# Optimization experiments

Measured on AMD Instinct MI355X. Metric: run time of the kernel, lower is better.

## Reference

```python
import jax, jax.numpy as jnp
import numpy as np

WINDOW = 25          # window_size -> h = w = 25, n = 625 tokens
DIM = 512
DIM_HEAD = 64
HEADS = DIM // DIM_HEAD
BATCH = 64


def _rel_pos_indices(ws):
    # mirrors the torch buffer: pairwise relative offsets on a ws x ws grid
    pos = np.arange(ws)
    gi, gj = np.meshgrid(pos, pos, indexing='ij')
    grid = np.stack([gi.reshape(-1), gj.reshape(-1)], axis=-1)      # (ws*ws, 2)
    rel = grid[:, None, :] - grid[None, :, :] + (ws - 1)            # (n, n, 2)
    return (rel[..., 0] * (2 * ws - 1) + rel[..., 1]).astype(np.int32)


def setup_inputs() -> dict:
    key = jax.random.key(0)
    k1, k2, k3, k4 = jax.random.split(key, 4)
    x = jax.random.normal(k1, (BATCH, DIM, WINDOW, WINDOW), jnp.float32)
    w_qkv = jax.random.normal(k2, (DIM, 3 * DIM), jnp.float32) * 0.02   # to_qkv weight (x @ w_qkv)
    w_out = jax.random.normal(k3, (DIM, DIM), jnp.float32) * 0.02       # to_out weight
    rel_pos_bias = jax.random.normal(k4, ((2 * WINDOW - 1) ** 2, HEADS), jnp.float32) * 0.02
    rel_pos_indices = jnp.asarray(_rel_pos_indices(WINDOW))
    return {"x": x, "w_qkv": w_qkv, "w_out": w_out,
            "rel_pos_bias": rel_pos_bias, "rel_pos_indices": rel_pos_indices}


def reference(x, w_qkv, w_out, rel_pos_bias, rel_pos_indices):
    b, d, h, w = x.shape
    n = h * w
    dh = DIM_HEAD
    m = d // dh
    scale = dh ** -0.5
    tokens = x.reshape(b, d, n).transpose(0, 2, 1)                  # b n d
    qkv = tokens @ w_qkv                                            # b n 3d
    q, k, v = jnp.split(qkv, 3, axis=-1)
    split_heads = lambda t: t.reshape(b, n, m, dh).transpose(0, 2, 1, 3)  # b m n dh
    q = split_heads(q) * scale
    k = split_heads(k)
    v = split_heads(v)
    sim = jnp.einsum('bmid,bmjd->bmij', q, k)                       # b m n n
    bias = rel_pos_bias[rel_pos_indices]                            # n n m  (embedding lookup)
    sim = sim + bias.transpose(2, 0, 1)[None]                       # add rel-pos bias inline
    attn = jax.nn.softmax(sim, axis=-1)
    out = jnp.einsum('bmij,bmjd->bmid', attn, v)                    # b m n dh
    out = out.transpose(0, 2, 1, 3).reshape(b, n, m * dh)           # concat heads
    out = out @ w_out                                               # b n d
    return out.transpose(0, 2, 1).reshape(b, d, h, w)
```

## Files before the change

kernel.cpp:

```cpp
#include <hip/hip_runtime.h>
#include <cstdint>
#include <cstddef>

typedef unsigned short u16;
typedef __attribute__((ext_vector_type(8))) short bf16x8;
typedef __attribute__((ext_vector_type(4))) float f32x4;

#define NB    64
#define NTOK  625
#define NTOKP 640
#define DDIM  512
#define NH    8
#define DH    64

__device__ __forceinline__ float bf2f(u16 v) {
    return __uint_as_float(((unsigned int)v) << 16);
}
__device__ __forceinline__ u16 f2bf(float f) {
    unsigned int x = __float_as_uint(f);
    unsigned int r = (x + 0x7fffu + ((x >> 16) & 1u)) >> 16;
    return (u16)r;
}
__device__ __forceinline__ u16 f2bf_fast(float f) {
    return (u16)((__float_as_uint(f) + 0x8000u) >> 16);
}

#if __has_builtin(__builtin_amdgcn_global_load_lds)
typedef const __attribute__((address_space(1))) void gas_void;
typedef __attribute__((address_space(3))) void las_void;
__device__ __forceinline__ void glds16(const void* g, void* l) {
    __builtin_amdgcn_global_load_lds((gas_void*)g, (las_void*)l, 16, 0, 0);
}
#else
__device__ __forceinline__ void glds16(const void* g, void* l) {
    *(uint4*)l = *(const uint4*)g;
}
#endif

__global__ __launch_bounds__(256) void k_transpose_x(const float* __restrict__ x,
                                                     u16* __restrict__ tokens) {
    __shared__ u16 T[64][66];
    int b = blockIdx.z, ct = blockIdx.y, it = blockIdx.x;
    int t = threadIdx.x;
    int i0 = it * 64, c0 = ct * 64;
#pragma unroll
    for (int r = 0; r < 2; r++) {
        int c = (t >> 3) + r * 32;
        int i8 = (t & 7) * 8;
        const float* s = x + ((size_t)b * DDIM + c0 + c) * NTOK + i0 + i8;
#pragma unroll
        for (int u = 0; u < 8; u++)
            T[c][i8 + u] = (i0 + i8 + u < NTOK) ? f2bf(s[u]) : (u16)0;
    }
    __syncthreads();
#pragma unroll
    for (int r = 0; r < 2; r++) {
        int i = (t >> 3) + r * 32;
        int c8 = (t & 7) * 8;
        int gi = i0 + i;
        u16* d = tokens + ((size_t)b * NTOKP + gi) * DDIM + c0 + c8;
#pragma unroll
        for (int u = 0; u < 8; u++) d[u] = T[c8 + u][i];
    }
}

__global__ __launch_bounds__(256) void k_transpose_w(const float* __restrict__ src,
                                                     u16* __restrict__ dst, int R, int C) {
    __shared__ u16 T[64][66];
    int r0 = blockIdx.y * 64, c0 = blockIdx.x * 64;
    int t = threadIdx.x;
#pragma unroll
    for (int rr = 0; rr < 2; rr++) {
        int r = (t >> 3) + rr * 32;
        int c8 = (t & 7) * 8;
        const float* s = src + (size_t)(r0 + r) * C + c0 + c8;
#pragma unroll
        for (int u = 0; u < 8; u++) T[r][c8 + u] = f2bf(s[u]);
    }
    __syncthreads();
#pragma unroll
    for (int rr = 0; rr < 2; rr++) {
        int c = (t >> 3) + rr * 32;
        int r8 = (t & 7) * 8;
        u16* d = dst + (size_t)(c0 + c) * R + r0 + r8;
#pragma unroll
        for (int u = 0; u < 8; u++) d[u] = T[r8 + u][c];
    }
}

__global__ __launch_bounds__(256) void k_bias(const int* __restrict__ rpi,
                                              const float* __restrict__ rpb,
                                              float* __restrict__ biasCf) {
    int blk = blockIdx.x;
    int m = blk / 100, jt = (blk / 10) % 10, it = blk % 10;
    int t = threadIdx.x;
    float vals[16];
#pragma unroll
    for (int jj = 0; jj < 4; jj++) {
        int gj = jt * 64 + jj * 16 + (t & 15);
#pragma unroll
        for (int r = 0; r < 4; r++) {
            int gi = it * 64 + (t >> 6) * 16 + ((t >> 4) & 3) * 4 + r;
            float v;
            if (gj >= NTOK) v = -1e30f;
            else if (gi >= NTOK) v = 0.f;
            else v = rpb[rpi[gi * NTOK + gj] * NH + m];
            vals[jj * 4 + r] = v;
        }
    }
    float* d = biasCf + ((size_t)(m * 10 + jt) * 10 + it) * 4096 + t * 16;
#pragma unroll
    for (int g = 0; g < 4; g++)
        *(f32x4*)(d + g * 4) = *(f32x4*)&vals[g * 4];
}

__global__ __launch_bounds__(256, 4) void k_qkv(const u16* __restrict__ tokens,
                                                const u16* __restrict__ wT,
                                                u16* __restrict__ qk, u16* __restrict__ vT) {
    __shared__ u16 SMEM[9216];
    int bid = blockIdx.x;
    int c8id = bid & 7, t2 = bid >> 3;
    int jt = t2 % 12, q_ = t2 / 12;
    int itb = q_ * 8 + c8id;
    int it = itb % 5, b = itb / 5;
    int i0 = it * 128, j0 = jt * 128;
    int t = threadIdx.x;
    int w = t >> 6, lane = t & 63, quad = lane >> 4, l15 = lane & 15;
    int wr = w >> 1, wc = w & 1;
    int swl = (l15 + (l15 >> 2)) & 3;
    f32x4 acc[4][4] = {};
    const u16* abase = tokens + ((size_t)b * NTOKP + i0) * DDIM;
    const u16* bbase = wT + (size_t)j0 * DDIM;
    for (int k0 = 0; k0 < DDIM; k0 += 32) {
        __syncthreads();
#pragma unroll
        for (int c = 0; c < 2; c++) {
            int unit = c * 256 + t;
            int row = unit >> 2, cc = unit & 3;
            int gcol = (cc ^ ((row + (row >> 2)) & 3)) * 8;
            glds16(abase + (size_t)row * DDIM + k0 + gcol, SMEM + unit * 8);
            glds16(bbase + (size_t)row * DDIM + k0 + gcol, SMEM + 4096 + unit * 8);
        }
        __syncthreads();
        bf16x8 af[4], bfv[4];
        int chA = (quad ^ swl) * 8;
#pragma unroll
        for (int q2 = 0; q2 < 4; q2++) {
            af[q2]  = *(const bf16x8*)&SMEM[(wr * 64 + q2 * 16 + l15) * 32 + chA];
            bfv[q2] = *(const bf16x8*)&SMEM[4096 + (wc * 64 + q2 * 16 + l15) * 32 + chA];
        }
#pragma unroll
        for (int ii = 0; ii < 4; ii++)
#pragma unroll
            for (int jj = 0; jj < 4; jj++)
                acc[ii][jj] = __builtin_amdgcn_mfma_f32_16x16x32_bf16(af[ii], bfv[jj], acc[ii][jj], 0, 0, 0);
    }
    __syncthreads();
    if (jt < 8) {
        float scale = (j0 < 512) ? 0.125f : 1.0f;
#pragma unroll
        for (int h = 0; h < 2; h++) {
            if (h) __syncthreads();
            if (wr == h) {
#pragma unroll
                for (int ii = 0; ii < 4; ii++)
#pragma unroll
                    for (int jj = 0; jj < 4; jj++)
#pragma unroll
                        for (int r = 0; r < 4; r++)
                            SMEM[(ii * 16 + quad * 4 + r) * 136 + wc * 64 + jj * 16 + l15] =
                                f2bf(acc[ii][jj][r] * scale);
            }
            __syncthreads();
#pragma unroll
            for (int g = 0; g < 4; g++) {
                int unit = g * 256 + t;
                int tok = unit >> 4, ch8 = (unit & 15) * 8;
                *(uint4*)(qk + ((size_t)b * NTOKP + i0 + h * 64 + tok) * 1024 + j0 + ch8) =
                    *(uint4*)&SMEM[tok * 136 + ch8];
            }
        }
    } else {
        int ch0 = j0 - 1024;
#pragma unroll
        for (int h = 0; h < 2; h++) {
            if (h) __syncthreads();
            if (wr == h) {
#pragma unroll
                for (int ii = 0; ii < 4; ii++)
#pragma unroll
                    for (int jj = 0; jj < 4; jj++)
#pragma unroll
                        for (int r = 0; r < 4; r++) {
                            int tok = ii * 16 + quad * 4 + r;
                            SMEM[(wc * 64 + jj * 16 + l15) * 72 + (tok & 15) * 4 + (tok >> 4)] =
                                f2bf(acc[ii][jj][r]);
                        }
            }
            __syncthreads();
#pragma unroll
            for (int g = 0; g < 4; g++) {
                int unit = g * 256 + t;
                int chl = unit >> 3, tok8 = (unit & 7) * 8;
                int chv = ch0 + chl, hd = chv >> 6, tc = chv & 63;
                *(uint4*)(vT + (((size_t)b * NH + hd) * DH + tc) * NTOKP + i0 + h * 64 + tok8) =
                    *(uint4*)&SMEM[chl * 72 + tok8];
            }
        }
    }
}

__global__ __launch_bounds__(256) void k_attn(const u16* __restrict__ qk,
                                              const u16* __restrict__ vT,
                                              const float* __restrict__ biasCf,
                                              u16* __restrict__ attnout) {
    __shared__ u16 Qs[64][72];
    __shared__ u16 Ks[64][72];
    __shared__ u16 Vs[80][72];
    __shared__ u16 Ps[64][72];
    int bid = blockIdx.x;
    int c8id = bid & 7, t2 = bid >> 3;
    int it = t2 % 10, q_ = t2 / 10;
    int bm = q_ * 8 + c8id;
    int m = bm & 7, b = bm >> 3;
    int i0 = it * 64;
    int t = threadIdx.x;
    int w = t >> 6, lane = t & 63, quad = lane >> 4, l15 = lane & 15;
    {
        int row = 64 + (t >> 4), c4 = (t & 15) * 4;
        *(uint2*)&Vs[row][c4] = make_uint2(0x3F803F80u, 0x3F803F80u);
    }
#pragma unroll
    for (int r = 0; r < 2; r++) {
        int row = (t >> 3) + r * 32;
        int t8 = (t & 7) * 8;
        *(uint4*)&Qs[row][t8] =
            *(const uint4*)(qk + ((size_t)b * NTOKP + i0 + row) * 1024 + m * DH + t8);
    }
    __syncthreads();
    bf16x8 aq[2], vones[2];
#pragma unroll
    for (int kk = 0; kk < 2; kk++) {
        aq[kk]    = *(const bf16x8*)&Qs[w * 16 + l15][kk * 32 + quad * 8];
        vones[kk] = *(const bf16x8*)&Vs[64 + l15][kk * 32 + quad * 8];
    }
    f32x4 oacc[5] = {};
    const u16* vbase = vT + ((size_t)b * NH + m) * DH * NTOKP;
    const float* bC = biasCf + (size_t)(m * 100 + it) * 4096 + t * 16;

    for (int jt = 0; jt < 10; jt++) {
        int j0 = jt * 64;
        __syncthreads();
#pragma unroll
        for (int r = 0; r < 2; r++) {
            int row = (t >> 3) + r * 32;
            int c8 = (t & 7) * 8;
            *(uint4*)&Ks[row][c8] =
                *(const uint4*)(qk + ((size_t)b * NTOKP + j0 + row) * 1024 + 512 + m * DH + c8);
            *(uint4*)&Vs[row][c8] = *(const uint4*)(vbase + (size_t)row * NTOKP + j0 + c8);
        }
        __syncthreads();
        const float* bp = bC + (size_t)jt * 10 * 4096;
        f32x4 s[4];
#pragma unroll
        for (int jj = 0; jj < 4; jj++) s[jj] = *(const f32x4*)(bp + jj * 4);
#pragma unroll
        for (int jj = 0; jj < 4; jj++)
#pragma unroll
            for (int kk = 0; kk < 2; kk++) {
                bf16x8 bk = *(const bf16x8*)&Ks[jj * 16 + l15][kk * 32 + quad * 8];
                s[jj] = __builtin_amdgcn_mfma_f32_16x16x32_bf16(aq[kk], bk, s[jj], 0, 0, 0);
            }
#pragma unroll
        for (int r = 0; r < 4; r++) {
            float p0 = __expf(s[0][r]), p1 = __expf(s[1][r]);
            float p2 = __expf(s[2][r]), p3 = __expf(s[3][r]);
            uint2 pk;
            pk.x = (unsigned)f2bf_fast(p0) | ((unsigned)f2bf_fast(p1) << 16);
            pk.y = (unsigned)f2bf_fast(p2) | ((unsigned)f2bf_fast(p3) << 16);
            *(uint2*)&Ps[w * 16 + quad * 4 + r][l15 * 4] = pk;
        }
        bf16x8 ap[2];
#pragma unroll
        for (int kk = 0; kk < 2; kk++)
            ap[kk] = *(const bf16x8*)&Ps[w * 16 + l15][kk * 32 + quad * 8];
#pragma unroll
        for (int tt = 0; tt < 4; tt++)
#pragma unroll
            for (int kk = 0; kk < 2; kk++) {
                bf16x8 bv = *(const bf16x8*)&Vs[tt * 16 + l15][kk * 32 + quad * 8];
                oacc[tt] = __builtin_amdgcn_mfma_f32_16x16x32_bf16(ap[kk], bv, oacc[tt], 0, 0, 0);
            }
#pragma unroll
        for (int kk = 0; kk < 2; kk++)
            oacc[4] = __builtin_amdgcn_mfma_f32_16x16x32_bf16(ap[kk], vones[kk], oacc[4], 0, 0, 0);
    }
    float rinv[4];
#pragma unroll
    for (int r = 0; r < 4; r++) rinv[r] = __frcp_rn(oacc[4][r]);
#pragma unroll
    for (int tt = 0; tt < 4; tt++)
#pragma unroll
        for (int r = 0; r < 4; r++) {
            int gi = i0 + w * 16 + quad * 4 + r;
            if (gi < NTOK)
                attnout[((size_t)b * NTOKP + gi) * DDIM + m * DH + tt * 16 + l15] =
                    f2bf(oacc[tt][r] * rinv[r]);
        }
}

__global__ __launch_bounds__(256, 4) void k_out(const u16* __restrict__ attnout,
                                                const u16* __restrict__ woT,
                                                float* __restrict__ out) {
    __shared__ u16 SMEM[8192];
    int bid = blockIdx.x;
    int c8id = bid & 7, t2 = bid >> 3;
    int jt = t2 % 4, q_ = t2 / 4;
    int itb = q_ * 8 + c8id;
    int it = itb % 5, b = itb / 5;
    int j0 = jt * 128, i0 = it * 128;
    int t = threadIdx.x;
    int w = t >> 6, lane = t & 63, quad = lane >> 4, l15 = lane & 15;
    int wr = w >> 1, wc = w & 1;
    int swl = (l15 + (l15 >> 2)) & 3;
    f32x4 acc[4][4] = {};
    const u16* abase = woT + (size_t)j0 * DDIM;
    const u16* bbase = attnout + ((size_t)b * NTOKP + i0) * DDIM;
    for (int k0 = 0; k0 < DDIM; k0 += 32) {
        __syncthreads();
#pragma unroll
        for (int c = 0; c < 2; c++) {
            int unit = c * 256 + t;
            int row = unit >> 2, cc = unit & 3;
            int gcol = (cc ^ ((row + (row >> 2)) & 3)) * 8;
            glds16(abase + (size_t)row * DDIM + k0 + gcol, SMEM + unit * 8);
            glds16(bbase + (size_t)row * DDIM + k0 + gcol, SMEM + 4096 + unit * 8);
        }
        __syncthreads();
        bf16x8 af[4], bfv[4];
        int chA = (quad ^ swl) * 8;
#pragma unroll
        for (int q2 = 0; q2 < 4; q2++) {
            af[q2]  = *(const bf16x8*)&SMEM[(wr * 64 + q2 * 16 + l15) * 32 + chA];
            bfv[q2] = *(const bf16x8*)&SMEM[4096 + (wc * 64 + q2 * 16 + l15) * 32 + chA];
        }
#pragma unroll
        for (int ii = 0; ii < 4; ii++)
#pragma unroll
            for (int jj = 0; jj < 4; jj++)
                acc[ii][jj] = __builtin_amdgcn_mfma_f32_16x16x32_bf16(af[ii], bfv[jj], acc[ii][jj], 0, 0, 0);
    }
#pragma unroll
    for (int ii = 0; ii < 4; ii++)
#pragma unroll
        for (int jj = 0; jj < 4; jj++) {
            int gi = i0 + wc * 64 + jj * 16 + l15;
            if (gi >= NTOK) continue;
#pragma unroll
            for (int r = 0; r < 4; r++) {
                int gj = j0 + wr * 64 + ii * 16 + quad * 4 + r;
                out[((size_t)b * DDIM + gj) * NTOK + gi] = acc[ii][jj][r];
            }
        }
}

extern "C" void kernel_launch(void* const* d_in, const int* in_sizes, int n_in,
                              void* d_out, int out_size, void* d_ws, size_t ws_size,
                              hipStream_t stream) {
    const float* x    = (const float*)d_in[0];
    const float* wqkv = (const float*)d_in[1];
    const float* wout = (const float*)d_in[2];
    const float* rpb  = (const float*)d_in[3];
    const int*   rpi  = (const int*)d_in[4];
    float* out = (float*)d_out;

    char* ws = (char*)d_ws;
    size_t off = 0;
    auto alloc = [&](size_t nbytes) -> void* {
        void* p = ws + off;
        off += (nbytes + 255) & ~(size_t)255;
        return p;
    };
    u16* tokens   = (u16*)alloc((size_t)NB * NTOKP * DDIM * 2);
    u16* qk       = (u16*)alloc((size_t)NB * NTOKP * 1024 * 2);
    u16* vT       = (u16*)alloc((size_t)NB * NH * DH * NTOKP * 2);
    u16* wqkvT    = (u16*)alloc((size_t)1536 * DDIM * 2);
    u16* woutT    = (u16*)alloc((size_t)DDIM * DDIM * 2);
    float* biasCf = (float*)alloc((size_t)NH * 100 * 4096 * 4);
    u16* attnout  = tokens;

    k_transpose_x<<<dim3(10, 8, NB), 256, 0, stream>>>(x, tokens);
    k_transpose_w<<<dim3(1536 / 64, DDIM / 64), 256, 0, stream>>>(wqkv, wqkvT, DDIM, 1536);
    k_transpose_w<<<dim3(DDIM / 64, DDIM / 64), 256, 0, stream>>>(wout, woutT, DDIM, DDIM);
    k_bias<<<dim3(800), 256, 0, stream>>>(rpi, rpb, biasCf);
    k_qkv<<<dim3(3840), 256, 0, stream>>>(tokens, wqkvT, qk, vT);
    k_attn<<<dim3(5120), 256, 0, stream>>>(qk, vT, biasCf, attnout);
    k_out<<<dim3(1280), 256, 0, stream>>>(attnout, woutT, out);
}
```

Baseline: 419.5 us.

## Double-buffer LDS loads in GEMMs and attention, use exp2 with prescaled log2e

```diff
diff --git a/kernel.cpp b/kernel.cpp
--- a/kernel.cpp
+++ b/kernel.cpp
@@ -12,6 +12,7 @@
 #define DDIM  512
 #define NH    8
 #define DH    64
+#define LOG2E 1.44269504088896f
 
 __device__ __forceinline__ float bf2f(u16 v) {
     return __uint_as_float(((unsigned int)v) << 16);
@@ -21,8 +22,21 @@
     unsigned int r = (x + 0x7fffu + ((x >> 16) & 1u)) >> 16;
     return (u16)r;
 }
-__device__ __forceinline__ u16 f2bf_fast(float f) {
-    return (u16)((__float_as_uint(f) + 0x8000u) >> 16);
+__device__ __forceinline__ float fexp2(float x) {
+#if __has_builtin(__builtin_amdgcn_exp2f)
+    return __builtin_amdgcn_exp2f(x);
+#else
+    return exp2f(x);
+#endif
+}
+__device__ __forceinline__ unsigned pack_bf16(float a, float b) {
+#if __has_builtin(__builtin_amdgcn_perm)
+    return __builtin_amdgcn_perm(__float_as_uint(b) + 0x8000u,
+                                 __float_as_uint(a) + 0x8000u, 0x07060302u);
+#else
+    return ((__float_as_uint(a) + 0x8000u) >> 16) |
+           (((__float_as_uint(b) + 0x8000u) >> 16) << 16);
+#endif
 }
 
 #if __has_builtin(__builtin_amdgcn_global_load_lds)
@@ -105,7 +119,7 @@
             if (gj >= NTOK) v = -1e30f;
             else if (gi >= NTOK) v = 0.f;
             else v = rpb[rpi[gi * NTOK + gj] * NH + m];
-            vals[jj * 4 + r] = v;
+            vals[jj * 4 + r] = v * LOG2E;
         }
     }
     float* d = biasCf + ((size_t)(m * 10 + jt) * 10 + it) * 4096 + t * 16;
@@ -117,7 +131,7 @@
 __global__ __launch_bounds__(256, 4) void k_qkv(const u16* __restrict__ tokens,
                                                 const u16* __restrict__ wT,
                                                 u16* __restrict__ qk, u16* __restrict__ vT) {
-    __shared__ u16 SMEM[9216];
+    __shared__ u16 SMEM[16384];
     int bid = blockIdx.x;
     int c8id = bid & 7, t2 = bid >> 3;
     int jt = t2 % 12, q_ = t2 / 12;
@@ -128,36 +142,40 @@
     int w = t >> 6, lane = t & 63, quad = lane >> 4, l15 = lane & 15;
     int wr = w >> 1, wc = w & 1;
     int swl = (l15 + (l15 >> 2)) & 3;
-    f32x4 acc[4][4] = {};
     const u16* abase = tokens + ((size_t)b * NTOKP + i0) * DDIM;
     const u16* bbase = wT + (size_t)j0 * DDIM;
-    for (int k0 = 0; k0 < DDIM; k0 += 32) {
-        __syncthreads();
+    auto stage = [&](int k0, int buf) {
 #pragma unroll
         for (int c = 0; c < 2; c++) {
             int unit = c * 256 + t;
             int row = unit >> 2, cc = unit & 3;
             int gcol = (cc ^ ((row + (row >> 2)) & 3)) * 8;
-            glds16(abase + (size_t)row * DDIM + k0 + gcol, SMEM + unit * 8);
-            glds16(bbase + (size_t)row * DDIM + k0 + gcol, SMEM + 4096 + unit * 8);
-        }
-        __syncthreads();
+            glds16(abase + (size_t)row * DDIM + k0 + gcol, SMEM + buf * 4096 + unit * 8);
+            glds16(bbase + (size_t)row * DDIM + k0 + gcol, SMEM + 8192 + buf * 4096 + unit * 8);
+        }
+    };
+    stage(0, 0);
+    __syncthreads();
+    f32x4 acc[4][4] = {};
+    for (int k0 = 0; k0 < DDIM; k0 += 32) {
+        int pc = (k0 >> 5) & 1;
+        if (k0 + 32 < DDIM) stage(k0 + 32, pc ^ 1);
         bf16x8 af[4], bfv[4];
         int chA = (quad ^ swl) * 8;
 #pragma unroll
         for (int q2 = 0; q2 < 4; q2++) {
-            af[q2]  = *(const bf16x8*)&SMEM[(wr * 64 + q2 * 16 + l15) * 32 + chA];
-            bfv[q2] = *(const bf16x8*)&SMEM[4096 + (wc * 64 + q2 * 16 + l15) * 32 + chA];
+            af[q2]  = *(const bf16x8*)&SMEM[pc * 4096 + (wr * 64 + q2 * 16 + l15) * 32 + chA];
+            bfv[q2] = *(const bf16x8*)&SMEM[8192 + pc * 4096 + (wc * 64 + q2 * 16 + l15) * 32 + chA];
         }
 #pragma unroll
         for (int ii = 0; ii < 4; ii++)
 #pragma unroll
             for (int jj = 0; jj < 4; jj++)
                 acc[ii][jj] = __builtin_amdgcn_mfma_f32_16x16x32_bf16(af[ii], bfv[jj], acc[ii][jj], 0, 0, 0);
-    }
-    __syncthreads();
+        __syncthreads();
+    }
     if (jt < 8) {
-        float scale = (j0 < 512) ? 0.125f : 1.0f;
+        float scale = (j0 < 512) ? 0.125f * LOG2E : 1.0f;
 #pragma unroll
         for (int h = 0; h < 2; h++) {
             if (h) __syncthreads();
@@ -210,14 +228,11 @@
     }
 }
 
-__global__ __launch_bounds__(256) void k_attn(const u16* __restrict__ qk,
-                                              const u16* __restrict__ vT,
-                                              const float* __restrict__ biasCf,
-                                              u16* __restrict__ attnout) {
-    __shared__ u16 Qs[64][72];
-    __shared__ u16 Ks[64][72];
-    __shared__ u16 Vs[80][72];
-    __shared__ u16 Ps[64][72];
+__global__ __launch_bounds__(256, 3) void k_attn(const u16* __restrict__ qk,
+                                                 const u16* __restrict__ vT,
+                                                 const float* __restrict__ biasCf,
+                                                 u16* __restrict__ attnout) {
+    __shared__ u16 S[25088];
     int bid = blockIdx.x;
     int c8id = bid & 7, t2 = bid >> 3;
     int it = t2 % 10, q_ = t2 / 10;
@@ -226,74 +241,96 @@
     int i0 = it * 64;
     int t = threadIdx.x;
     int w = t >> 6, lane = t & 63, quad = lane >> 4, l15 = lane & 15;
-    {
-        int row = 64 + (t >> 4), c4 = (t & 15) * 4;
-        *(uint2*)&Vs[row][c4] = make_uint2(0x3F803F80u, 0x3F803F80u);
-    }
-#pragma unroll
-    for (int r = 0; r < 2; r++) {
-        int row = (t >> 3) + r * 32;
-        int t8 = (t & 7) * 8;
-        *(uint4*)&Qs[row][t8] =
-            *(const uint4*)(qk + ((size_t)b * NTOKP + i0 + row) * 1024 + m * DH + t8);
-    }
+
+    const u16* qbase = qk + ((size_t)b * NTOKP + i0) * 1024 + m * DH;
+    const u16* kbase = qk + (size_t)b * NTOKP * 1024 + 512 + m * DH;
+    const u16* vbase = vT + ((size_t)b * NH + m) * DH * NTOKP;
+
+#pragma unroll
+    for (int c = 0; c < 2; c++) {
+        int unit = c * 256 + t;
+        int row = unit >> 3, pch = unit & 7;
+        int gcol = (pch ^ (row & 7)) * 8;
+        glds16(qbase + (size_t)row * 1024 + gcol, S + unit * 8);
+    }
+#pragma unroll
+    for (int c = 0; c < 2; c++) {
+        int unit = c * 256 + t;
+        int row = unit >> 3, pch = unit & 7;
+        int gcol = (pch ^ (row & 7)) * 8;
+        glds16(kbase + (size_t)row * 1024 + gcol, S + 4096 + unit * 8);
+        glds16(vbase + (size_t)row * NTOKP + gcol, S + 12288 + unit * 8);
+    }
+    const float* bC = biasCf + (size_t)(m * 100 + it) * 4096 + t * 16;
+    f32x4 ba[2][4];
+#pragma unroll
+    for (int jj = 0; jj < 4; jj++) ba[0][jj] = *(const f32x4*)(bC + jj * 4);
     __syncthreads();
-    bf16x8 aq[2], vones[2];
-#pragma unroll
-    for (int kk = 0; kk < 2; kk++) {
-        aq[kk]    = *(const bf16x8*)&Qs[w * 16 + l15][kk * 32 + quad * 8];
-        vones[kk] = *(const bf16x8*)&Vs[64 + l15][kk * 32 + quad * 8];
-    }
+
+    bf16x8 aq[2];
+#pragma unroll
+    for (int kk = 0; kk < 2; kk++)
+        aq[kk] = *(const bf16x8*)&S[(w * 16 + l15) * 64 + ((4 * kk + quad) ^ (l15 & 7)) * 8];
+    bf16x8 vone;
+#pragma unroll
+    for (int e = 0; e < 8; e++) vone[e] = (short)0x3F80;
+
     f32x4 oacc[5] = {};
-    const u16* vbase = vT + ((size_t)b * NH + m) * DH * NTOKP;
-    const float* bC = biasCf + (size_t)(m * 100 + it) * 4096 + t * 16;
-
+#pragma unroll
     for (int jt = 0; jt < 10; jt++) {
-        int j0 = jt * 64;
+        int p = jt & 1;
+        if (jt < 9) {
+            const float* bp = bC + (size_t)(jt + 1) * 40960;
+#pragma unroll
+            for (int jj = 0; jj < 4; jj++) ba[p ^ 1][jj] = *(const f32x4*)(bp + jj * 4);
+            int j1 = (jt + 1) * 64;
+#pragma unroll
+            for (int c = 0; c < 2; c++) {
+                int unit = c * 256 + t;
+                int row = unit >> 3, pch = unit & 7;
+                int gcol = (pch ^ (row & 7)) * 8;
+                glds16(kbase + (size_t)(j1 + row) * 1024 + gcol,
+                       S + 4096 + (p ^ 1) * 4096 + unit * 8);
+                glds16(vbase + (size_t)row * NTOKP + j1 + gcol,
+                       S + 12288 + (p ^ 1) * 4096 + unit * 8);
+            }
+        }
+        f32x4 s[4];
+#pragma unroll
+        for (int jj = 0; jj < 4; jj++) s[jj] = ba[p][jj];
+#pragma unroll
+        for (int jj = 0; jj < 4; jj++)
+#pragma unroll
+            for (int kk = 0; kk < 2; kk++) {
+                bf16x8 bk = *(const bf16x8*)&S[4096 + p * 4096 + (jj * 16 + l15) * 64 +
+                                               ((4 * kk + quad) ^ (l15 & 7)) * 8];
+                s[jj] = __builtin_amdgcn_mfma_f32_16x16x32_bf16(aq[kk], bk, s[jj], 0, 0, 0);
+            }
+#pragma unroll
+        for (int r = 0; r < 4; r++) {
+            float p0 = fexp2(s[0][r]), p1 = fexp2(s[1][r]);
+            float p2 = fexp2(s[2][r]), p3 = fexp2(s[3][r]);
+            uint2 pk;
+            pk.x = pack_bf16(p0, p1);
+            pk.y = pack_bf16(p2, p3);
+            *(uint2*)&S[20480 + (w * 16 + quad * 4 + r) * 72 + l15 * 4] = pk;
+        }
+        bf16x8 ap[2];
+#pragma unroll
+        for (int kk = 0; kk < 2; kk++)
+            ap[kk] = *(const bf16x8*)&S[20480 + (w * 16 + l15) * 72 + kk * 32 + quad * 8];
+#pragma unroll
+        for (int tt = 0; tt < 4; tt++)
+#pragma unroll
+            for (int kk = 0; kk < 2; kk++) {
+                bf16x8 bv = *(const bf16x8*)&S[12288 + p * 4096 + (tt * 16 + l15) * 64 +
+                                               ((4 * kk + quad) ^ (l15 & 7)) * 8];
+                oacc[tt] = __builtin_amdgcn_mfma_f32_16x16x32_bf16(ap[kk], bv, oacc[tt], 0, 0, 0);
+            }
+#pragma unroll
+        for (int kk = 0; kk < 2; kk++)
+            oacc[4] = __builtin_amdgcn_mfma_f32_16x16x32_bf16(ap[kk], vone, oacc[4], 0, 0, 0);
         __syncthreads();
-#pragma unroll
-        for (int r = 0; r < 2; r++) {
-            int row = (t >> 3) + r * 32;
-            int c8 = (t & 7) * 8;
-            *(uint4*)&Ks[row][c8] =
-                *(const uint4*)(qk + ((size_t)b * NTOKP + j0 + row) * 1024 + 512 + m * DH + c8);
-            *(uint4*)&Vs[row][c8] = *(const uint4*)(vbase + (size_t)row * NTOKP + j0 + c8);
-        }
-        __syncthreads();
-        const float* bp = bC + (size_t)jt * 10 * 4096;
-        f32x4 s[4];
-#pragma unroll
-        for (int jj = 0; jj < 4; jj++) s[jj] = *(const f32x4*)(bp + jj * 4);
-#pragma unroll
-        for (int jj = 0; jj < 4; jj++)
-#pragma unroll
-            for (int kk = 0; kk < 2; kk++) {
-                bf16x8 bk = *(const bf16x8*)&Ks[jj * 16 + l15][kk * 32 + quad * 8];
-                s[jj] = __builtin_amdgcn_mfma_f32_16x16x32_bf16(aq[kk], bk, s[jj], 0, 0, 0);
-            }
-#pragma unroll
-        for (int r = 0; r < 4; r++) {
-            float p0 = __expf(s[0][r]), p1 = __expf(s[1][r]);
-            float p2 = __expf(s[2][r]), p3 = __expf(s[3][r]);
-            uint2 pk;
-            pk.x = (unsigned)f2bf_fast(p0) | ((unsigned)f2bf_fast(p1) << 16);
-            pk.y = (unsigned)f2bf_fast(p2) | ((unsigned)f2bf_fast(p3) << 16);
-            *(uint2*)&Ps[w * 16 + quad * 4 + r][l15 * 4] = pk;
-        }
-        bf16x8 ap[2];
-#pragma unroll
-        for (int kk = 0; kk < 2; kk++)
-            ap[kk] = *(const bf16x8*)&Ps[w * 16 + l15][kk * 32 + quad * 8];
-#pragma unroll
-        for (int tt = 0; tt < 4; tt++)
-#pragma unroll
-            for (int kk = 0; kk < 2; kk++) {
-                bf16x8 bv = *(const bf16x8*)&Vs[tt * 16 + l15][kk * 32 + quad * 8];
-                oacc[tt] = __builtin_amdgcn_mfma_f32_16x16x32_bf16(ap[kk], bv, oacc[tt], 0, 0, 0);
-            }
-#pragma unroll
-        for (int kk = 0; kk < 2; kk++)
-            oacc[4] = __builtin_amdgcn_mfma_f32_16x16x32_bf16(ap[kk], vones[kk], oacc[4], 0, 0, 0);
     }
     float rinv[4];
 #pragma unroll
@@ -312,7 +349,7 @@
 __global__ __launch_bounds__(256, 4) void k_out(const u16* __restrict__ attnout,
                                                 const u16* __restrict__ woT,
                                                 float* __restrict__ out) {
-    __shared__ u16 SMEM[8192];
+    __shared__ u16 SMEM[16384];
     int bid = blockIdx.x;
     int c8id = bid & 7, t2 = bid >> 3;
     int jt = t2 % 4, q_ = t2 / 4;
@@ -323,32 +360,37 @@
     int w = t >> 6, lane = t & 63, quad = lane >> 4, l15 = lane & 15;
     int wr = w >> 1, wc = w & 1;
     int swl = (l15 + (l15 >> 2)) & 3;
-    f32x4 acc[4][4] = {};
     const u16* abase = woT + (size_t)j0 * DDIM;
     const u16* bbase = attnout + ((size_t)b * NTOKP + i0) * DDIM;
-    for (int k0 = 0; k0 < DDIM; k0 += 32) {
-        __syncthreads();
+    auto stage = [&](int k0, int buf) {
 #pragma unroll
         for (int c = 0; c < 2; c++) {
             int unit = c * 256 + t;
             int row = unit >> 2, cc = unit & 3;
             int gcol = (cc ^ ((row + (row >> 2)) & 3)) * 8;
-            glds16(abase + (size_t)row * DDIM + k0 + gcol, SMEM + unit * 8);
-            glds16(bbase + (size_t)row * DDIM + k0 + gcol, SMEM + 4096 + unit * 8);
-        }
-        __syncthreads();
+            glds16(abase + (size_t)row * DDIM + k0 + gcol, SMEM + buf * 4096 + unit * 8);
+            glds16(bbase + (size_t)row * DDIM + k0 + gcol, SMEM + 8192 + buf * 4096 + unit * 8);
+        }
+    };
+    stage(0, 0);
+    __syncthreads();
+    f32x4 acc[4][4] = {};
+    for (int k0 = 0; k0 < DDIM; k0 += 32) {
+        int pc = (k0 >> 5) & 1;
+        if (k0 + 32 < DDIM) stage(k0 + 32, pc ^ 1);
         bf16x8 af[4], bfv[4];
         int chA = (quad ^ swl) * 8;
 #pragma unroll
         for (int q2 = 0; q2 < 4; q2++) {
-            af[q2]  = *(const bf16x8*)&SMEM[(wr * 64 + q2 * 16 + l15) * 32 + chA];
-            bfv[q2] = *(const bf16x8*)&SMEM[4096 + (wc * 64 + q2 * 16 + l15) * 32 + chA];
+            af[q2]  = *(const bf16x8*)&SMEM[pc * 4096 + (wr * 64 + q2 * 16 + l15) * 32 + chA];
+            bfv[q2] = *(const bf16x8*)&SMEM[8192 + pc * 4096 + (wc * 64 + q2 * 16 + l15) * 32 + chA];
         }
 #pragma unroll
         for (int ii = 0; ii < 4; ii++)
 #pragma unroll
             for (int jj = 0; jj < 4; jj++)
                 acc[ii][jj] = __builtin_amdgcn_mfma_f32_16x16x32_bf16(af[ii], bfv[jj], acc[ii][jj], 0, 0, 0);
+        __syncthreads();
     }
 #pragma unroll
     for (int ii = 0; ii < 4; ii++)
```

Result: faster. 409.2 us (-2.5%).
